# Kernel optimization log

Measured on AMD Instinct MI355X. Metric: run time of the kernel, lower is better.

The kernel has to match this reference:

```python
import jax, jax.numpy as jnp
import numpy as np

DIM = 1024
HEADS = 16
DIM_HEAD = DIM // HEADS  # 64
MAX_FREQ = 256


def rotate_half(x):
    # interleaved pairs: (..., d) -> rotate each (x1, x2) pair to (-x2, x1)
    x = x.reshape(*x.shape[:-1], -1, 2)
    x1, x2 = x[..., 0], x[..., 1]
    return jnp.stack([-x2, x1], axis=-1).reshape(*x.shape[:-2], -1)


def axial_freqs_2d(H, W, rot_dim, max_freq):
    # 'pixel' freqs: linspace(1, max_freq/2, n) * pi per axis; each axis gets rot_dim/2 rotary dims
    n = rot_dim // 4
    freqs = jnp.linspace(1.0, max_freq / 2.0, n, dtype=jnp.float32) * jnp.pi
    ph = jnp.linspace(-1.0, 1.0, H, dtype=jnp.float32)
    pw = jnp.linspace(-1.0, 1.0, W, dtype=jnp.float32)
    fh = jnp.repeat(ph[:, None] * freqs[None, :], 2, axis=-1)  # (H, rot_dim//2)
    fw = jnp.repeat(pw[:, None] * freqs[None, :], 2, axis=-1)  # (W, rot_dim//2)
    fh = jnp.broadcast_to(fh[:, None, :], (H, W, rot_dim // 2))
    fw = jnp.broadcast_to(fw[None, :, :], (H, W, rot_dim // 2))
    return jnp.concatenate([fh, fw], axis=-1)  # (H, W, rot_dim)


def setup_inputs() -> dict:
    key = jax.random.key(0)
    k1, k2, k3 = jax.random.split(key, 3)
    b, H, W = 8, 32, 32
    L = H * W
    x = jax.random.normal(k1, (b, L, DIM), dtype=jnp.float32)
    # torch Linear weights stored pre-transposed for direct x @ W
    w_qkv = jax.random.normal(k2, (DIM, 3 * DIM), dtype=jnp.float32) * (DIM ** -0.5)
    w_proj = jax.random.normal(k3, (DIM, DIM), dtype=jnp.float32) * (DIM ** -0.5)
    return {"x": x, "w_qkv": w_qkv, "w_proj": w_proj, "H": H, "W": W}


def reference(x, w_qkv, w_proj, H, W):
    b, L, d = x.shape
    qkv = x @ w_qkv  # (b, L, 3d)
    q, k, v = jnp.split(qkv, 3, axis=-1)

    def split_heads(t):
        return t.reshape(b, L, HEADS, DIM_HEAD)  # (b, L, h, dh)

    q, k, v = split_heads(q), split_heads(k), split_heads(v)

    # 2D axial RoPE over the full head dim (rope_use_dim == dim_head)
    freqs = axial_freqs_2d(H, W, DIM_HEAD, MAX_FREQ).reshape(L, DIM_HEAD)
    cos = jnp.cos(freqs)[None, :, None, :]  # (1, L, 1, dh)
    sin = jnp.sin(freqs)[None, :, None, :]
    q = q * cos + rotate_half(q) * sin
    k = k * cos + rotate_half(k) * sin

    # module pre-scales q by dh^-0.5 AND SDPA scales again by dh^-0.5 -> dh^-1 total (faithful)
    scale_total = 1.0 / DIM_HEAD
    scores = jnp.einsum('blhd,bmhd->bhlm', q, k) * scale_total  # (b, h, L, L)
    attn = jax.nn.softmax(scores, axis=-1)
    out = jnp.einsum('bhlm,bmhd->blhd', attn, v).reshape(b, L, d)
    return out @ w_proj
```

## Files before the change

### kernel.cpp

```cpp
#include <hip/hip_runtime.h>
#include <hip/hip_bf16.h>
#include <math.h>

typedef __bf16 bf16_t;
typedef __attribute__((ext_vector_type(8))) __bf16 bf16x8;
typedef __attribute__((ext_vector_type(4))) __bf16 bf16x4;
typedef __attribute__((ext_vector_type(4))) short s16x4;
typedef __attribute__((ext_vector_type(4))) float f32x4;

#define AS1C(p) ((const __attribute__((address_space(1))) void*)(p))
#define AS3(p)  ((__attribute__((address_space(3))) void*)(p))

__device__ __forceinline__ float fast_exp2(float x) { return __builtin_amdgcn_exp2f(x); }

__device__ __forceinline__ void tconv_body(const float* __restrict__ in,
                                           bf16_t* __restrict__ out, int R, int C,
                                           int r0, int c0, float (*tile)[65], int tid) {
#pragma unroll
    for (int i = 0; i < 16; ++i) {
        int e = i * 256 + tid;
        int r = e >> 6, c = e & 63;
        tile[r][c] = in[(size_t)(r0 + r) * C + c0 + c];
    }
    __syncthreads();
#pragma unroll
    for (int i = 0; i < 16; ++i) {
        int e = i * 256 + tid;
        int c = e >> 6, r = e & 63;
        out[(size_t)(c0 + c) * R + r0 + r] = (bf16_t)tile[r][c];
    }
}

__global__ __launch_bounds__(256) void k_prep(const float* __restrict__ x,
                                              const float* __restrict__ wqkv,
                                              const float* __restrict__ wproj,
                                              bf16_t* __restrict__ xb,
                                              bf16_t* __restrict__ wqT,
                                              bf16_t* __restrict__ wpT,
                                              float* __restrict__ cosT,
                                              float* __restrict__ sinT) {
    __shared__ float tile[64][65];
    const int bid = blockIdx.x, tid = threadIdx.x;
    if (bid < 8192) {
        int i = bid * 256 + tid;
        float4 v = reinterpret_cast<const float4*>(x)[i];
        bf16x4 o;
        o[0] = (bf16_t)v.x; o[1] = (bf16_t)v.y; o[2] = (bf16_t)v.z; o[3] = (bf16_t)v.w;
        reinterpret_cast<bf16x4*>(xb)[i] = o;
    } else if (bid < 8960) {
        int t = bid - 8192;
        tconv_body(wqkv, wqT, 1024, 3072, (t / 48) * 64, (t % 48) * 64, tile, tid);
    } else if (bid < 9216) {
        int t = bid - 8960;
        tconv_body(wproj, wpT, 1024, 1024, (t / 16) * 64, (t % 16) * 64, tile, tid);
    } else {
        int i = (bid - 9216) * 256 + tid;
        int l = i >> 6, d = i & 63;
        int hh = l >> 5, ww = l & 31;
        float pos = (d < 32) ? (-1.0f + (2.0f / 31.0f) * (float)hh)
                             : (-1.0f + (2.0f / 31.0f) * (float)ww);
        int fi = (d & 31) >> 1;
        float fb = (1.0f + (127.0f / 15.0f) * (float)fi) * 3.14159265358979323846f;
        float fr = pos * fb;
        cosT[i] = cosf(fr);
        sinT[i] = sinf(fr);
    }
}

__device__ __forceinline__ void gemm128_pipe(const bf16_t* __restrict__ A,
                                             const bf16_t* __restrict__ Bt,
                                             int rowA0, int colB0, int w, int l,
                                             bf16_t* As, bf16_t* Bs,
                                             f32x4 acc[4][4]) {
    const int wr = w >> 1, wc = w & 1;
    const int r8 = l >> 3;
    const int sc = ((l & 7) ^ r8) << 3;

#define STG8(buf, kt)                                                                      \
    {                                                                                      \
        _Pragma("unroll")                                                                  \
        for (int j = 0; j < 4; ++j) {                                                      \
            int rr = j * 32 + w * 8 + r8;                                                  \
            __builtin_amdgcn_global_load_lds(                                              \
                AS1C(A + (size_t)(rowA0 + rr) * 1024 + (kt) * 64 + sc),                    \
                AS3(As + (buf) * 8192 + (j * 32 + w * 8) * 64), 16, 0, 0);                 \
            __builtin_amdgcn_global_load_lds(                                              \
                AS1C(Bt + (size_t)(colB0 + rr) * 1024 + (kt) * 64 + sc),                   \
                AS3(Bs + (buf) * 8192 + (j * 32 + w * 8) * 64), 16, 0, 0);                 \
        }                                                                                  \
    }

    STG8(0, 0);
    for (int T = 0; T < 16; ++T) {
        if (T < 15) {
            STG8((T + 1) & 1, T + 1);
            asm volatile("s_waitcnt vmcnt(8)" ::: "memory");
        } else {
            asm volatile("s_waitcnt vmcnt(0)" ::: "memory");
        }
        __builtin_amdgcn_s_barrier();
        const bf16_t* cA = As + (T & 1) * 8192;
        const bf16_t* cB = Bs + (T & 1) * 8192;
#pragma unroll
        for (int kk = 0; kk < 2; ++kk) {
            const int ec = (kk * 32 + (l >> 4) * 8) ^ ((l & 7) << 3);
            bf16x8 af[4], bfr[4];
#pragma unroll
            for (int mm = 0; mm < 4; ++mm)
                af[mm] = *reinterpret_cast<const bf16x8*>(
                    cA + (wr * 64 + mm * 16 + (l & 15)) * 64 + ec);
#pragma unroll
            for (int n = 0; n < 4; ++n)
                bfr[n] = *reinterpret_cast<const bf16x8*>(
                    cB + (wc * 64 + n * 16 + (l & 15)) * 64 + ec);
            asm volatile("s_waitcnt lgkmcnt(0)" ::: "memory");
            __builtin_amdgcn_sched_barrier(0);
            __builtin_amdgcn_s_setprio(1);
#pragma unroll
            for (int mm = 0; mm < 4; ++mm)
#pragma unroll
                for (int n = 0; n < 4; ++n)
                    acc[mm][n] = __builtin_amdgcn_mfma_f32_16x16x32_bf16(af[mm], bfr[n],
                                                                         acc[mm][n], 0, 0, 0);
            __builtin_amdgcn_s_setprio(0);
        }
        __builtin_amdgcn_s_barrier();
    }
#undef STG8
}

__global__ __launch_bounds__(256, 2) void k_gemm_qkv(const bf16_t* __restrict__ A,
                                                     const bf16_t* __restrict__ Bt,
                                                     const float* __restrict__ cosT,
                                                     const float* __restrict__ sinT,
                                                     bf16_t* __restrict__ qb,
                                                     bf16_t* __restrict__ kb,
                                                     bf16_t* __restrict__ vb) {
    __shared__ alignas(128) char smem[65536];
    bf16_t* As = (bf16_t*)smem;
    bf16_t* Bs = (bf16_t*)(smem + 32768);
    const int tid = threadIdx.x, w = tid >> 6, l = tid & 63;
    const int wr = w >> 1, wc = w & 1;
    const int bid = blockIdx.x;
    const int xcd = bid & 7, idx = bid >> 3;
    const int by = (xcd >> 1) * 16 + (idx & 15);
    const int bx = (xcd & 1) * 12 + (idx >> 4);
    const int rowA0 = by * 128, colB0 = bx * 128;

    f32x4 acc[4][4] = {};
    gemm128_pipe(A, Bt, rowA0, colB0, w, l, As, Bs, acc);

    const int part = colB0 >> 10;
    if (part == 2) {
        __builtin_amdgcn_sched_barrier(0);
        __syncthreads();
        bf16_t* Tb = (bf16_t*)smem;
#pragma unroll
        for (int m = 0; m < 4; ++m)
#pragma unroll
            for (int n = 0; n < 4; ++n) {
                int cc = wc * 64 + n * 16 + (l & 15);
                int rr = wr * 64 + m * 16 + (l >> 4) * 4;
#pragma unroll
                for (int r = 0; r < 4; ++r)
                    Tb[cc * 136 + rr + r] = (bf16_t)acc[m][n][r];
            }
        __syncthreads();
        const int j = tid >> 1, half = tid & 1;
        const int c = colB0 + j;
        const int head = (c & 1023) >> 6, d = c & 63;
        const int bb = rowA0 >> 10, ll0 = rowA0 & 1023;
        bf16_t* dst = vb + (((size_t)bb * 16 + head) * 64 + d) * 1024 + ll0 + half * 64;
        const bf16_t* srcp = Tb + j * 136 + half * 64;
#pragma unroll
        for (int e = 0; e < 8; ++e)
            *reinterpret_cast<bf16x8*>(dst + e * 8) =
                *reinterpret_cast<const bf16x8*>(srcp + e * 8);
    } else {
        bf16_t* dstb = (part == 0) ? qb : kb;
#pragma unroll
        for (int m = 0; m < 4; ++m)
#pragma unroll
            for (int n = 0; n < 4; ++n) {
                const int c = colB0 + wc * 64 + n * 16 + (l & 15);
                const int head = (c & 1023) >> 6;
                const int d = c & 63;
                const int rbase = rowA0 + wr * 64 + m * 16 + (l >> 4) * 4;
#pragma unroll
                for (int r = 0; r < 4; ++r) {
                    int row = rbase + r;
                    int bb = row >> 10, ll = row & 1023;
                    float v0 = acc[m][n][r];
                    float vp = __shfl_xor(v0, 1, 64);
                    float cs = cosT[ll * 64 + d];
                    float sn = sinT[ll * 64 + d];
                    float res = (d & 1) ? fmaf(vp, sn, v0 * cs) : fmaf(-vp, sn, v0 * cs);
                    dstb[(((size_t)bb * 16 + head) * 1024 + ll) * 64 + d] = (bf16_t)res;
                }
            }
    }
}

__global__ __launch_bounds__(256, 2) void k_gemm_out(const bf16_t* __restrict__ A,
                                                     const bf16_t* __restrict__ Bt,
                                                     float* __restrict__ out) {
    __shared__ alignas(128) char smem[65536];
    bf16_t* As = (bf16_t*)smem;
    bf16_t* Bs = (bf16_t*)(smem + 32768);
    const int tid = threadIdx.x, w = tid >> 6, l = tid & 63;
    const int wr = w >> 1, wc = w & 1;
    const int bid = blockIdx.x;
    const int xcd = bid & 7, idx = bid >> 3;
    const int by = (xcd >> 1) * 16 + (idx & 15);
    const int bx = (xcd & 1) * 4 + (idx >> 4);
    const int rowA0 = by * 128, colB0 = bx * 128;

    f32x4 acc[4][4] = {};
    gemm128_pipe(A, Bt, rowA0, colB0, w, l, As, Bs, acc);

#pragma unroll
    for (int m = 0; m < 4; ++m)
#pragma unroll
        for (int n = 0; n < 4; ++n) {
            int c = colB0 + wc * 64 + n * 16 + (l & 15);
            int rbase = rowA0 + wr * 64 + m * 16 + (l >> 4) * 4;
#pragma unroll
            for (int r = 0; r < 4; ++r)
                out[(size_t)(rbase + r) * 1024 + c] = acc[m][n][r];
        }
}

__global__ __launch_bounds__(512, 4) void k_attn(const bf16_t* __restrict__ qb,
                                                 const bf16_t* __restrict__ kb,
                                                 const bf16_t* __restrict__ vb,
                                                 bf16_t* __restrict__ ob) {
    __shared__ alignas(128) bf16_t Ks[2][64 * 64];
    __shared__ alignas(128) bf16_t Vs[2][64 * 64];
    const int tid = threadIdx.x, w = tid >> 6, l = tid & 63;
    const int g = l >> 4;
    const int bid = blockIdx.x;
    const int bs = (bid & 7) * 64 + (bid >> 3);
    const int bh = bs >> 2, bi = bh >> 4, h = bh & 15;
    const int q0 = (bs & 3) * 256;
    const bf16_t* qbase = qb + (size_t)bh * 1024 * 64;
    const bf16_t* kbase = kb + (size_t)bh * 1024 * 64;
    const bf16_t* vbase = vb + (size_t)bh * 64 * 1024;

    bf16x8 qf[2][2];
#pragma unroll
    for (int m = 0; m < 2; ++m) {
        int qrow = q0 + w * 32 + m * 16 + (l & 15);
#pragma unroll
        for (int kk = 0; kk < 2; ++kk)
            qf[m][kk] = *reinterpret_cast<const bf16x8*>(
                qbase + (size_t)qrow * 64 + kk * 32 + g * 8);
    }

    float m_run[2] = {-1e30f, -1e30f};
    float l_run[2] = {0.f, 0.f};
    f32x4 o_acc[2][4] = {};

    const int srow = l >> 3;
    const int sc = 8 * ((l & 7) ^ srow);
#define STAGE(buf, kv0)                                                                   \
    {                                                                                     \
        int rr = w * 8 + srow;                                                            \
        __builtin_amdgcn_global_load_lds(AS1C(kbase + (size_t)((kv0) + rr) * 64 + sc),    \
                                         AS3(&Ks[buf][w * 512]), 16, 0, 0);               \
        __builtin_amdgcn_global_load_lds(AS1C(vbase + (size_t)rr * 1024 + (kv0) + sc),    \
                                         AS3(&Vs[buf][w * 512]), 16, 0, 0);               \
    }

    STAGE(0, 0);
    __syncthreads();

    const float SCL = 1.4426950408889634f / 64.0f;
    int cur = 0;
    for (int t = 0; t < 16; ++t) {
        if (t < 15) STAGE(cur ^ 1, (t + 1) * 64);

        f32x4 sacc[2][4] = {};
#pragma unroll
        for (int kk = 0; kk < 2; ++kk)
#pragma unroll
            for (int n = 0; n < 4; ++n) {
                int rr = n * 16 + (l & 15);
                int ec = (kk * 32 + g * 8) ^ ((l & 7) << 3);
                bf16x8 kfr = *reinterpret_cast<const bf16x8*>(&Ks[cur][rr * 64 + ec]);
                sacc[0][n] = __builtin_amdgcn_mfma_f32_16x16x32_bf16(kfr, qf[0][kk], sacc[0][n], 0, 0, 0);
                sacc[1][n] = __builtin_amdgcn_mfma_f32_16x16x32_bf16(kfr, qf[1][kk], sacc[1][n], 0, 0, 0);
            }

        s16x4 pa[2][4];
#pragma unroll
        for (int m = 0; m < 2; ++m) {
            float mxr = -1e30f;
#pragma unroll
            for (int n = 0; n < 4; ++n)
#pragma unroll
                for (int r = 0; r < 4; ++r) mxr = fmaxf(mxr, sacc[m][n][r]);
            mxr = fmaxf(mxr, __shfl_xor(mxr, 16, 64));
            mxr = fmaxf(mxr, __shfl_xor(mxr, 32, 64));
            float mx = mxr * SCL;
            float mo = m_run[m];
            if (__any(mx > mo + 8.0f)) {
                float mn = fmaxf(mo, mx);
                float corr = fast_exp2(mo - mn);
                l_run[m] *= corr;
                m_run[m] = mn; mo = mn;
#pragma unroll
                for (int r = 0; r < 4; ++r) {
                    float c2 = __shfl(corr, (l & 48) | (g * 4 + r), 64);
#pragma unroll
                    for (int n = 0; n < 4; ++n) o_acc[m][n][r] *= c2;
                }
            }
            float lsum = 0.f;
#pragma unroll
            for (int n = 0; n < 4; ++n) {
                bf16x4 pb;
#pragma unroll
                for (int r = 0; r < 4; ++r) {
                    float pv = fast_exp2(fmaf(sacc[m][n][r], SCL, -mo));
                    lsum += pv;
                    pb[r] = (bf16_t)pv;
                }
                pa[m][n] = __builtin_bit_cast(s16x4, pb);
            }
            l_run[m] += lsum;
        }

        const char* vrow = (const char*)&Vs[cur][0] + (l & 15) * 128;
#pragma unroll
        for (int c = 0; c < 4; ++c) {
            int kvb = (c * 32 + g * 8) ^ ((l & 7) << 4);
#pragma unroll
            for (int nd = 0; nd < 4; ++nd) {
                s16x4 vf = *reinterpret_cast<const s16x4*>(vrow + nd * 2048 + kvb);
                o_acc[0][nd] = __builtin_amdgcn_mfma_f32_16x16x16bf16_1k(pa[0][c], vf, o_acc[0][nd], 0, 0, 0);
                o_acc[1][nd] = __builtin_amdgcn_mfma_f32_16x16x16bf16_1k(pa[1][c], vf, o_acc[1][nd], 0, 0, 0);
            }
        }
        __syncthreads();
        cur ^= 1;
    }

#pragma unroll
    for (int m = 0; m < 2; ++m) {
        float ls = l_run[m];
        ls += __shfl_xor(ls, 16, 64);
        ls += __shfl_xor(ls, 32, 64);
        float inv = 1.0f / ls;
#pragma unroll
        for (int r = 0; r < 4; ++r) {
            float c2 = __shfl(inv, (l & 48) | (g * 4 + r), 64);
            int row = q0 + w * 32 + m * 16 + g * 4 + r;
#pragma unroll
            for (int n = 0; n < 4; ++n)
                ob[((size_t)bi * 1024 + row) * 1024 + h * 64 + n * 16 + (l & 15)] =
                    (bf16_t)(o_acc[m][n][r] * c2);
        }
    }
#undef STAGE
}

extern "C" void kernel_launch(void* const* d_in, const int* in_sizes, int n_in,
                              void* d_out, int out_size, void* d_ws, size_t ws_size,
                              hipStream_t stream) {
    (void)in_sizes; (void)n_in; (void)out_size; (void)ws_size;
    const float* x     = (const float*)d_in[0];
    const float* wqkv  = (const float*)d_in[1];
    const float* wproj = (const float*)d_in[2];
    char* ws = (char*)d_ws;

    bf16_t* xb  = (bf16_t*)(ws);
    bf16_t* wqT = (bf16_t*)(ws + 16777216ull);
    bf16_t* wpT = (bf16_t*)(ws + 23068672ull);
    bf16_t* qb  = (bf16_t*)(ws + 25165824ull);
    bf16_t* kb  = (bf16_t*)(ws + 41943040ull);
    bf16_t* vb  = (bf16_t*)(ws + 58720256ull);
    bf16_t* ob  = (bf16_t*)(ws + 75497472ull);
    float*  cosT = (float*)(ws + 92274688ull);
    float*  sinT = (float*)(ws + 92536832ull);

    k_prep<<<9472, 256, 0, stream>>>(x, wqkv, wproj, xb, wqT, wpT, cosT, sinT);
    k_gemm_qkv<<<1536, 256, 0, stream>>>(xb, wqT, cosT, sinT, qb, kb, vb);
    k_attn<<<512, 512, 0, stream>>>(qb, kb, vb, ob);
    k_gemm_out<<<512, 256, 0, stream>>>(ob, wpT, (float*)d_out);
}
```

Baseline: 154.7 us.

## Enlarge GEMM tiles to 256x128 with 8 waves and triple-buffered LDS pipeline

Both projection GEMMs now use 256x128 output tiles computed by 512-thread blocks (8 waves), with a three-stage LDS ring buffer that prefetches three k-steps ahead instead of double buffering. The grid is halved and the block-to-tile mapping is redone so each XCD covers a contiguous row band. The V transpose epilogue is widened to the taller tile. This aims to raise operand reuse per global load and hide more memory latency. In exchange it uses 144 KB of LDS, which allows only one block per CU, and it halves the number of blocks.

```diff
diff --git a/kernel.cpp b/kernel.cpp
--- a/kernel.cpp
+++ b/kernel.cpp
@@ -67,7 +67,7 @@
     }
 }
 
-__device__ __forceinline__ void gemm128_pipe(const bf16_t* __restrict__ A,
+__device__ __forceinline__ void gemm256_pipe(const bf16_t* __restrict__ A,
                                              const bf16_t* __restrict__ Bt,
                                              int rowA0, int colB0, int w, int l,
                                              bf16_t* As, bf16_t* Bs,
@@ -76,31 +76,32 @@
     const int r8 = l >> 3;
     const int sc = ((l & 7) ^ r8) << 3;
 
-#define STG8(buf, kt)                                                                      \
+#define STG6(buf, kt)                                                                      \
     {                                                                                      \
         _Pragma("unroll")                                                                  \
-        for (int j = 0; j < 4; ++j) {                                                      \
-            int rr = j * 32 + w * 8 + r8;                                                  \
+        for (int j = 0; j < 4; ++j)                                                        \
             __builtin_amdgcn_global_load_lds(                                              \
-                AS1C(A + (size_t)(rowA0 + rr) * 1024 + (kt) * 64 + sc),                    \
-                AS3(As + (buf) * 8192 + (j * 32 + w * 8) * 64), 16, 0, 0);                 \
+                AS1C(A + (size_t)(rowA0 + j * 64 + w * 8 + r8) * 1024 + (kt) * 64 + sc),   \
+                AS3(As + (buf) * 16384 + (j * 64 + w * 8) * 64), 16, 0, 0);                \
+        _Pragma("unroll")                                                                  \
+        for (int j = 0; j < 2; ++j)                                                        \
             __builtin_amdgcn_global_load_lds(                                              \
-                AS1C(Bt + (size_t)(colB0 + rr) * 1024 + (kt) * 64 + sc),                   \
-                AS3(Bs + (buf) * 8192 + (j * 32 + w * 8) * 64), 16, 0, 0);                 \
-        }                                                                                  \
-    }
-
-    STG8(0, 0);
+                AS1C(Bt + (size_t)(colB0 + j * 64 + w * 8 + r8) * 1024 + (kt) * 64 + sc),  \
+                AS3(Bs + (buf) * 8192 + (j * 64 + w * 8) * 64), 16, 0, 0);                 \
+    }
+
+    STG6(0, 0);
+    STG6(1, 1);
+    STG6(2, 2);
+
+    int cur = 0;
     for (int T = 0; T < 16; ++T) {
-        if (T < 15) {
-            STG8((T + 1) & 1, T + 1);
-            asm volatile("s_waitcnt vmcnt(8)" ::: "memory");
-        } else {
-            asm volatile("s_waitcnt vmcnt(0)" ::: "memory");
-        }
+        if (T <= 13)      asm volatile("s_waitcnt vmcnt(12)" ::: "memory");
+        else if (T == 14) asm volatile("s_waitcnt vmcnt(6)" ::: "memory");
+        else              asm volatile("s_waitcnt vmcnt(0)" ::: "memory");
         __builtin_amdgcn_s_barrier();
-        const bf16_t* cA = As + (T & 1) * 8192;
-        const bf16_t* cB = Bs + (T & 1) * 8192;
+        const bf16_t* cA = As + cur * 16384;
+        const bf16_t* cB = Bs + cur * 8192;
 #pragma unroll
         for (int kk = 0; kk < 2; ++kk) {
             const int ec = (kk * 32 + (l >> 4) * 8) ^ ((l & 7) << 3);
@@ -125,30 +126,32 @@
             __builtin_amdgcn_s_setprio(0);
         }
         __builtin_amdgcn_s_barrier();
-    }
-#undef STG8
-}
-
-__global__ __launch_bounds__(256, 2) void k_gemm_qkv(const bf16_t* __restrict__ A,
+        if (T < 13) STG6(cur, T + 3);
+        cur = (cur == 2) ? 0 : cur + 1;
+    }
+#undef STG6
+}
+
+__global__ __launch_bounds__(512, 1) void k_gemm_qkv(const bf16_t* __restrict__ A,
                                                      const bf16_t* __restrict__ Bt,
                                                      const float* __restrict__ cosT,
                                                      const float* __restrict__ sinT,
                                                      bf16_t* __restrict__ qb,
                                                      bf16_t* __restrict__ kb,
                                                      bf16_t* __restrict__ vb) {
-    __shared__ alignas(128) char smem[65536];
+    __shared__ alignas(128) char smem[147456];
     bf16_t* As = (bf16_t*)smem;
-    bf16_t* Bs = (bf16_t*)(smem + 32768);
+    bf16_t* Bs = (bf16_t*)(smem + 98304);
     const int tid = threadIdx.x, w = tid >> 6, l = tid & 63;
     const int wr = w >> 1, wc = w & 1;
     const int bid = blockIdx.x;
     const int xcd = bid & 7, idx = bid >> 3;
-    const int by = (xcd >> 1) * 16 + (idx & 15);
-    const int bx = (xcd & 1) * 12 + (idx >> 4);
-    const int rowA0 = by * 128, colB0 = bx * 128;
+    const int by = xcd * 4 + (idx & 3);
+    const int bx = idx >> 2;
+    const int rowA0 = by * 256, colB0 = bx * 128;
 
     f32x4 acc[4][4] = {};
-    gemm128_pipe(A, Bt, rowA0, colB0, w, l, As, Bs, acc);
+    gemm256_pipe(A, Bt, rowA0, colB0, w, l, As, Bs, acc);
 
     const int part = colB0 >> 10;
     if (part == 2) {
@@ -163,15 +166,15 @@
                 int rr = wr * 64 + m * 16 + (l >> 4) * 4;
 #pragma unroll
                 for (int r = 0; r < 4; ++r)
-                    Tb[cc * 136 + rr + r] = (bf16_t)acc[m][n][r];
+                    Tb[cc * 264 + rr + r] = (bf16_t)acc[m][n][r];
             }
         __syncthreads();
-        const int j = tid >> 1, half = tid & 1;
+        const int j = tid >> 2, qtr = tid & 3;
         const int c = colB0 + j;
         const int head = (c & 1023) >> 6, d = c & 63;
         const int bb = rowA0 >> 10, ll0 = rowA0 & 1023;
-        bf16_t* dst = vb + (((size_t)bb * 16 + head) * 64 + d) * 1024 + ll0 + half * 64;
-        const bf16_t* srcp = Tb + j * 136 + half * 64;
+        bf16_t* dst = vb + (((size_t)bb * 16 + head) * 64 + d) * 1024 + ll0 + qtr * 64;
+        const bf16_t* srcp = Tb + j * 264 + qtr * 64;
 #pragma unroll
         for (int e = 0; e < 8; ++e)
             *reinterpret_cast<bf16x8*>(dst + e * 8) =
@@ -201,22 +204,22 @@
     }
 }
 
-__global__ __launch_bounds__(256, 2) void k_gemm_out(const bf16_t* __restrict__ A,
+__global__ __launch_bounds__(512, 1) void k_gemm_out(const bf16_t* __restrict__ A,
                                                      const bf16_t* __restrict__ Bt,
                                                      float* __restrict__ out) {
-    __shared__ alignas(128) char smem[65536];
+    __shared__ alignas(128) char smem[147456];
     bf16_t* As = (bf16_t*)smem;
-    bf16_t* Bs = (bf16_t*)(smem + 32768);
+    bf16_t* Bs = (bf16_t*)(smem + 98304);
     const int tid = threadIdx.x, w = tid >> 6, l = tid & 63;
     const int wr = w >> 1, wc = w & 1;
     const int bid = blockIdx.x;
     const int xcd = bid & 7, idx = bid >> 3;
-    const int by = (xcd >> 1) * 16 + (idx & 15);
-    const int bx = (xcd & 1) * 4 + (idx >> 4);
-    const int rowA0 = by * 128, colB0 = bx * 128;
+    const int by = xcd * 4 + (idx & 3);
+    const int bx = idx >> 2;
+    const int rowA0 = by * 256, colB0 = bx * 128;
 
     f32x4 acc[4][4] = {};
-    gemm128_pipe(A, Bt, rowA0, colB0, w, l, As, Bs, acc);
+    gemm256_pipe(A, Bt, rowA0, colB0, w, l, As, Bs, acc);
 
 #pragma unroll
     for (int m = 0; m < 4; ++m)
@@ -384,7 +387,7 @@
     float*  sinT = (float*)(ws + 92536832ull);
 
     k_prep<<<9472, 256, 0, stream>>>(x, wqkv, wproj, xb, wqT, wpT, cosT, sinT);
-    k_gemm_qkv<<<1536, 256, 0, stream>>>(xb, wqT, cosT, sinT, qb, kb, vb);
+    k_gemm_qkv<<<768, 512, 0, stream>>>(xb, wqT, cosT, sinT, qb, kb, vb);
     k_attn<<<512, 512, 0, stream>>>(qb, kb, vb, ob);
-    k_gemm_out<<<512, 256, 0, stream>>>(ob, wpT, (float*)d_out);
-}
+    k_gemm_out<<<256, 512, 0, stream>>>(ob, wpT, (float*)d_out);
+}
```

Measured after the change: 157.7 us. Within noise of the previous version (+1.9%).
